# Kernel tuning notes

Hardware: AMD Instinct MI355X
Metric: run time of the kernel (lower is better)

Reference implementation:

```python
import jax, jax.numpy as jnp
import numpy as np

KH, KW = 5, 5  # filter_size
PAD_H, PAD_W = KH // 2, KW // 2


def setup_inputs() -> dict:
    key = jax.random.key(0)
    k1, k2 = jax.random.split(key)
    n, c, h, w = 4, 3, 180, 320
    filter_prod = KH * KW          # 25
    upsampling_square = 16
    x = jax.random.normal(k1, (n, c, h, w), dtype=jnp.float32)
    filters = jax.random.uniform(k2, (n, filter_prod, upsampling_square, h, w), dtype=jnp.float32)
    return {"x": x, "filters": filters}


def _unfold(x):
    # Equivalent of conv2d with a grouped identity (eye) expansion filter:
    # extracts kh*kw patches per channel in row-major (i, j) kernel order.
    n, c, h, w = x.shape
    xp = jnp.pad(x, ((0, 0), (0, 0), (PAD_H, PAD_H), (PAD_W, PAD_W)))
    # (n, c, kh*kw, h, w); fixed 25-iteration loop over kernel taps.
    patches = jnp.stack(
        [xp[:, :, i:i + h, j:j + w] for i in range(KH) for j in range(KW)],
        axis=2,
    )
    return patches


def reference(x, filters):
    n, filter_prod, upsampling_square, h, w = filters.shape
    patches = _unfold(x)  # (n, 3, filter_prod, h, w)
    out = jnp.einsum('ncphw,npuhw->ncuhw', patches, filters)
    return out.reshape(n, 3 * upsampling_square, h, w)
```

## Files before the change

### kernel.cpp

```cpp
#include <hip/hip_runtime.h>


#define HH 180
#define WW 320
#define CC 3
#define UU 16
#define NN 4
#define HP (HH + 4)
#define WP 328
#define HW (HH * WW)
#define PHW (HP * WP)

__global__ __launch_bounds__(256) void pad_x_kernel(
    const float* __restrict__ x, float* __restrict__ xpad)
{
    int idx = blockIdx.x * 256 + threadIdx.x;
    int wp = idx % WP;
    int t  = idx / WP;
    int hp = t % HP;
    int nc = t / HP;
    int h = hp - 2, w = wp - 2;
    float v = 0.f;
    if (h >= 0 && h < HH && w >= 0 && w < WW)
        v = x[(size_t)nc * HW + h * WW + w];
    xpad[idx] = v;
}

__global__ __launch_bounds__(256) void duf_kernel(
    const float* __restrict__ xpad,
    const float* __restrict__ filters,
    float* __restrict__ out)
{
    int idx = blockIdx.x * 256 + threadIdx.x;
    int w4 = idx % (WW / 4);
    int t  = idx / (WW / 4);
    int h  = t % HH;
    t /= HH;
    int u = t % UU;
    int n = t / UU;

    const int wbase = w4 * 4;
    const float* fptr = filters + (((size_t)n * 25 * UU + u) * HW + (size_t)h * WW + wbase);

    float acc[CC][4];
    #pragma unroll
    for (int c = 0; c < CC; ++c)
        #pragma unroll
        for (int q = 0; q < 4; ++q) acc[c][q] = 0.f;

    #pragma unroll
    for (int i = 0; i < 5; ++i) {
        float xv[CC][8];
        #pragma unroll
        for (int c = 0; c < CC; ++c) {
            const float* xr = xpad + ((size_t)(n * CC + c) * HP + (h + i)) * WP + wbase;
            float4 a = *(const float4*)xr;
            float4 b = *(const float4*)(xr + 4);
            xv[c][0] = a.x; xv[c][1] = a.y; xv[c][2] = a.z; xv[c][3] = a.w;
            xv[c][4] = b.x; xv[c][5] = b.y; xv[c][6] = b.z; xv[c][7] = b.w;
        }
        #pragma unroll
        for (int j = 0; j < 5; ++j) {
            float4 f = *(const float4*)(fptr + (size_t)(i * 5 + j) * UU * HW);
            #pragma unroll
            for (int c = 0; c < CC; ++c) {
                acc[c][0] += xv[c][j + 0] * f.x;
                acc[c][1] += xv[c][j + 1] * f.y;
                acc[c][2] += xv[c][j + 2] * f.z;
                acc[c][3] += xv[c][j + 3] * f.w;
            }
        }
    }

    #pragma unroll
    for (int c = 0; c < CC; ++c) {
        float* op = out + (((size_t)n * CC * UU + c * UU + u) * HW + (size_t)h * WW + wbase);
        *(float4*)op = make_float4(acc[c][0], acc[c][1], acc[c][2], acc[c][3]);
    }
}

extern "C" void kernel_launch(void* const* d_in, const int* in_sizes, int n_in,
                              void* d_out, int out_size, void* d_ws, size_t ws_size,
                              hipStream_t stream) {
    const float* x       = (const float*)d_in[0];
    const float* filters = (const float*)d_in[1];
    float* out           = (float*)d_out;
    float* xpad          = (float*)d_ws;

    const int pad_total = NN * CC * PHW;
    pad_x_kernel<<<pad_total / 256, 256, 0, stream>>>(x, xpad);

    const int total = NN * UU * HH * (WW / 4);
    duf_kernel<<<total / 256, 256, 0, stream>>>(xpad, filters, out);
}
```

Baseline: 496.6 us.

## Stage padded input row bands in shared memory per block

Each block now covers one (batch, upsample index, 4-row band) and cooperatively copies the 8 padded input rows for all 3 channels into LDS. Threads then read their 5x8 input windows from LDS instead of global memory, while the filter loads stay as before. The aim is to cut redundant global and L2 traffic for the input taps. In exchange, the block uses about 31 KB of LDS and adds a barrier before compute, which can lower occupancy and delay the filter loads.

```diff
diff --git a/kernel.cpp b/kernel.cpp
--- a/kernel.cpp
+++ b/kernel.cpp
@@ -9,7 +9,10 @@
 #define HP (HH + 4)
 #define WP 328
 #define HW (HH * WW)
-#define PHW (HP * WP)
+#define RB 4
+#define NBANDS (HH / RB)
+#define BT 320
+#define SLAB_ROWS (RB + 4)
 
 __global__ __launch_bounds__(256) void pad_x_kernel(
     const float* __restrict__ x, float* __restrict__ xpad)
@@ -26,21 +29,40 @@
     xpad[idx] = v;
 }
 
-__global__ __launch_bounds__(256) void duf_kernel(
+__global__ __launch_bounds__(BT) void duf_kernel(
     const float* __restrict__ xpad,
     const float* __restrict__ filters,
     float* __restrict__ out)
 {
-    int idx = blockIdx.x * 256 + threadIdx.x;
-    int w4 = idx % (WW / 4);
-    int t  = idx / (WW / 4);
-    int h  = t % HH;
-    t /= HH;
-    int u = t % UU;
-    int n = t / UU;
+    __shared__ float xl[CC * SLAB_ROWS * WP];
 
+    const int tid = threadIdx.x;
+    int b = blockIdx.x;
+    const int band = b % NBANDS;
+    int t = b / NBANDS;
+    const int u = t % UU;
+    const int n = t / UU;
+    const int h0 = band * RB;
+
+    {
+        const float* xsrc = xpad + ((size_t)n * CC * HP + h0) * WP;
+        const int groups = CC * SLAB_ROWS * (WP / 4);
+        for (int g = tid; g < groups; g += BT) {
+            int colg = g % (WP / 4);
+            int rr   = (g / (WP / 4)) % SLAB_ROWS;
+            int c    = g / (WP / 4) / SLAB_ROWS;
+            float4 v = *(const float4*)(xsrc + ((size_t)c * HP + rr) * WP + colg * 4);
+            *(float4*)(&xl[(c * SLAB_ROWS + rr) * WP + colg * 4]) = v;
+        }
+    }
+    __syncthreads();
+
+    const int w4 = tid % (WW / 4);
+    const int r  = tid / (WW / 4);
     const int wbase = w4 * 4;
-    const float* fptr = filters + (((size_t)n * 25 * UU + u) * HW + (size_t)h * WW + wbase);
+    const int flat = (h0 + r) * WW + wbase;
+
+    const float* fbase = filters + ((size_t)n * 25 * UU + u) * HW + flat;
 
     float acc[CC][4];
     #pragma unroll
@@ -53,15 +75,15 @@
         float xv[CC][8];
         #pragma unroll
         for (int c = 0; c < CC; ++c) {
-            const float* xr = xpad + ((size_t)(n * CC + c) * HP + (h + i)) * WP + wbase;
-            float4 a = *(const float4*)xr;
-            float4 b = *(const float4*)(xr + 4);
-            xv[c][0] = a.x; xv[c][1] = a.y; xv[c][2] = a.z; xv[c][3] = a.w;
-            xv[c][4] = b.x; xv[c][5] = b.y; xv[c][6] = b.z; xv[c][7] = b.w;
+            const float* ls = &xl[(c * SLAB_ROWS + r + i) * WP + wbase];
+            float4 a = *(const float4*)ls;
+            float4 bq = *(const float4*)(ls + 4);
+            xv[c][0] = a.x;  xv[c][1] = a.y;  xv[c][2] = a.z;  xv[c][3] = a.w;
+            xv[c][4] = bq.x; xv[c][5] = bq.y; xv[c][6] = bq.z; xv[c][7] = bq.w;
         }
         #pragma unroll
         for (int j = 0; j < 5; ++j) {
-            float4 f = *(const float4*)(fptr + (size_t)(i * 5 + j) * UU * HW);
+            float4 f = *(const float4*)(fbase + (size_t)(i * 5 + j) * UU * HW);
             #pragma unroll
             for (int c = 0; c < CC; ++c) {
                 acc[c][0] += xv[c][j + 0] * f.x;
@@ -72,11 +94,11 @@
         }
     }
 
+    float* ob = out + ((size_t)n * CC * UU + u) * HW + flat;
     #pragma unroll
-    for (int c = 0; c < CC; ++c) {
-        float* op = out + (((size_t)n * CC * UU + c * UU + u) * HW + (size_t)h * WW + wbase);
-        *(float4*)op = make_float4(acc[c][0], acc[c][1], acc[c][2], acc[c][3]);
-    }
+    for (int c = 0; c < CC; ++c)
+        *(float4*)(ob + (size_t)c * UU * HW) =
+            make_float4(acc[c][0], acc[c][1], acc[c][2], acc[c][3]);
 }
 
 extern "C" void kernel_launch(void* const* d_in, const int* in_sizes, int n_in,
@@ -87,9 +109,9 @@
     float* out           = (float*)d_out;
     float* xpad          = (float*)d_ws;
 
-    const int pad_total = NN * CC * PHW;
+    const int pad_total = NN * CC * HP * WP;
     pad_x_kernel<<<pad_total / 256, 256, 0, stream>>>(x, xpad);
 
-    const int total = NN * UU * HH * (WW / 4);
-    duf_kernel<<<total / 256, 256, 0, stream>>>(xpad, filters, out);
+    const int grid = NN * UU * NBANDS;
+    duf_kernel<<<grid, BT, 0, stream>>>(xpad, filters, out);
 }
```

New measurement: 498.6 us. No clear change (+0.4%).
